# Kernel tuning notes

Measured on AMD Instinct MI355X. Metric: run time of the kernel, lower is better.

The kernel has to match this reference:

```python
import jax, jax.numpy as jnp
import numpy as np
from jax import lax

D_MODEL = 512
N_HEADS = 8
D_HEAD = D_MODEL // N_HEADS
MAX_LANDMARKS = 100


def setup_inputs() -> dict:
    key = jax.random.key(0)
    ks = jax.random.split(key, 12)
    B, L, D = 16, 8192, D_MODEL
    s = 1.0 / np.sqrt(D)
    return {
        "mamba_output": jax.random.normal(ks[0], (B, L, D), jnp.float32),
        "hawkes_skip": jax.random.normal(ks[1], (B, L, D), jnp.float32),
        "hawkes_weights": jax.random.uniform(ks[2], (B, L), jnp.float32),
        "Wq": jax.random.uniform(ks[3], (D, D), jnp.float32, -s, s),
        "bq": jax.random.uniform(ks[4], (D,), jnp.float32, -s, s),
        "Wk": jax.random.uniform(ks[5], (D, D), jnp.float32, -s, s),
        "bk": jax.random.uniform(ks[6], (D,), jnp.float32, -s, s),
        "Wv": jax.random.uniform(ks[7], (D, D), jnp.float32, -s, s),
        "bv": jax.random.uniform(ks[8], (D,), jnp.float32, -s, s),
        "Wo": jax.random.uniform(ks[9], (D, D), jnp.float32, -s, s),
        "bo": jax.random.uniform(ks[10], (D,), jnp.float32, -s, s),
    }


def reference(mamba_output, hawkes_skip, hawkes_weights,
              Wq, bq, Wk, bk, Wv, bv, Wo, bo):
    B, L, D = hawkes_skip.shape
    H, dh = N_HEADS, D_HEAD
    k = min(MAX_LANDMARKS, L)
    scale = dh ** (-0.5)

    # top-k landmark selection over sequence, then chronological sort
    _, idx = lax.top_k(hawkes_weights, k)          # (B, k)
    idx = jnp.sort(idx, axis=1)
    landmark_kv = jnp.take_along_axis(hawkes_skip, idx[:, :, None], axis=1)  # (B, k, D)

    # single query = last timestep of mamba output
    query = mamba_output[:, -1, :]                 # (B, D)
    Q = (query @ Wq.T + bq).reshape(B, H, dh)      # (B, H, dh)
    K = (landmark_kv @ Wk.T + bk).reshape(B, k, H, dh)
    V = (landmark_kv @ Wv.T + bv).reshape(B, k, H, dh)

    scores = jnp.einsum("bhd,bkhd->bhk", Q, K) * scale   # (B, H, k)
    probs = jax.nn.softmax(scores, axis=-1)
    attn = jnp.einsum("bhk,bkhd->bhd", probs, V).reshape(B, D)
    return attn @ Wo.T + bo                        # (B, D)
```

## Files before the change

kernel.cpp:

```cpp
#include <hip/hip_runtime.h>
#include <hip/hip_bf16.h>
#include <stdint.h>

#define B_SZ 16
#define L_SEQ 8192
#define D_MOD 512
#define N_H 8
#define D_H 64
#define KSEL 100

__global__ __launch_bounds__(512) void fused_attn_kernel(
    const float* __restrict__ mamba, const float* __restrict__ skip,
    const float* __restrict__ w,
    const float* __restrict__ Wq, const float* __restrict__ bq,
    const float* __restrict__ Wk, const float* __restrict__ bk,
    const float* __restrict__ Wv, const float* __restrict__ bv,
    float* __restrict__ attn_out) {
    const int b = blockIdx.x >> 3;
    const int h = blockIdx.x & 7;
    const int t = threadIdx.x;
    const int lane = t & 63;
    const int wave = t >> 6;

    __shared__ uint32_t uval[L_SEQ];
    __shared__ float s_part[8 * D_MOD];
    __shared__ float s_query[D_MOD];
    __shared__ float s_a[D_MOD];
    __shared__ float s_y[D_MOD];
    __shared__ float s_Qh[D_H];
    __shared__ int s_idx[128];
    __shared__ int hist[256];
    __shared__ int s_wtot[4];
    __shared__ float s_m[8], s_l[8];
    __shared__ uint32_t s_thresh;
    __shared__ int s_rem, s_cnt;
    __shared__ float s_qdotbk;

    const float* qrow = mamba + ((size_t)b * L_SEQ + (L_SEQ - 1)) * D_MOD;
    if (t < D_MOD) s_query[t] = qrow[t];
    const float* wb = w + (size_t)b * L_SEQ;
    for (int i = t; i < L_SEQ; i += 512) uval[i] = __float_as_uint(wb[i]);
    __syncthreads();

    const float* Wqh = Wq + (size_t)(h * D_H) * D_MOD;
    {
        const float4* q4 = (const float4*)s_query;
        float4 q0 = q4[lane * 2], q1 = q4[lane * 2 + 1];
        for (int d = wave; d < D_H; d += 8) {
            const float4* row4 = (const float4*)(Wqh + (size_t)d * D_MOD);
            float4 w0 = row4[lane * 2], w1 = row4[lane * 2 + 1];
            float sum = w0.x * q0.x + w0.y * q0.y + w0.z * q0.z + w0.w * q0.w +
                        w1.x * q1.x + w1.y * q1.y + w1.z * q1.z + w1.w * q1.w;
            #pragma unroll
            for (int off = 32; off > 0; off >>= 1) sum += __shfl_down(sum, off);
            if (lane == 0) s_Qh[d] = sum + bq[h * D_H + d];
        }
    }
    __syncthreads();

    if (wave == 0) {
        float v = s_Qh[lane] * bk[h * D_H + lane];
        #pragma unroll
        for (int off = 32; off > 0; off >>= 1) v += __shfl_down(v, off);
        if (lane == 0) s_qdotbk = v;
    }
    {
        const float* Wkh = Wk + (size_t)(h * D_H) * D_MOD;
        float4 a0 = {0, 0, 0, 0}, a1 = {0, 0, 0, 0};
        #pragma unroll
        for (int dd = 0; dd < 8; ++dd) {
            const int d = wave * 8 + dd;
            float qd = s_Qh[d];
            const float4* row4 = (const float4*)(Wkh + (size_t)d * D_MOD);
            float4 w0 = row4[lane * 2], w1 = row4[lane * 2 + 1];
            a0.x += qd * w0.x; a0.y += qd * w0.y; a0.z += qd * w0.z; a0.w += qd * w0.w;
            a1.x += qd * w1.x; a1.y += qd * w1.y; a1.z += qd * w1.z; a1.w += qd * w1.w;
        }
        float4* p4 = (float4*)&s_part[wave * D_MOD + lane * 8];
        p4[0] = a0; p4[1] = a1;
    }
    __syncthreads();
    {
        float v = 0.f;
        #pragma unroll
        for (int ww = 0; ww < 8; ++ww) v += s_part[ww * D_MOD + t];
        s_a[t] = v;
    }

    uint32_t prefix = 0, pmask = 0;
    int remaining = KSEL;
    for (int pass = 0; pass < 4; ++pass) {
        const int shift = 24 - 8 * pass;
        if (t < 256) hist[t] = 0;
        __syncthreads();
        for (int i = t; i < L_SEQ; i += 512) {
            uint32_t u = uval[i];
            if ((u & pmask) == prefix) atomicAdd(&hist[(u >> shift) & 0xFF], 1);
        }
        __syncthreads();
        int v = 0;
        if (t < 256) {
            v = hist[t];
            #pragma unroll
            for (int off = 1; off < 64; off <<= 1) {
                int u = __shfl_down(v, off);
                if (lane + off < 64) v += u;
            }
            if (lane == 0) s_wtot[wave] = v;
        }
        __syncthreads();
        if (t < 256) {
            int hi = 0;
            for (int w2 = wave + 1; w2 < 4; ++w2) hi += s_wtot[w2];
            int suff = v + hi;
            int suff_next = suff - hist[t];
            if (suff >= remaining && suff_next < remaining) {
                s_thresh = prefix | ((uint32_t)t << shift);
                s_rem = remaining - suff_next;
            }
        }
        __syncthreads();
        prefix = s_thresh;
        remaining = s_rem;
        pmask |= (uint32_t)0xFF << shift;
        __syncthreads();
    }

    if (t == 0) s_cnt = 0;
    __syncthreads();
    for (int i = t; i < L_SEQ; i += 512) {
        if (uval[i] > prefix) {
            int p = atomicAdd(&s_cnt, 1);
            s_idx[p] = i;
        }
    }
    __syncthreads();
    const int cntgt = s_cnt;
    if (wave == 0) {
        int needed = remaining;
        int taken = 0;
        for (int base = 0; base < L_SEQ && needed > 0; base += 64) {
            bool eq = (uval[base + lane] == prefix);
            unsigned long long mask = __ballot(eq);
            int before = __popcll(mask & ((1ull << lane) - 1ull));
            int c = __popcll(mask);
            int take = c < needed ? c : needed;
            if (eq && before < take) s_idx[cntgt + taken + before] = base + lane;
            taken += take;
            needed -= take;
        }
    }
    __syncthreads();

    const float scale = 0.125f;
    {
        const float4* a4 = (const float4*)s_a;
        float4 av0 = a4[lane * 2], av1 = a4[lane * 2 + 1];
        float qdotbk = s_qdotbk;
        float m = -INFINITY, l = 0.f;
        float4 acc0 = {0, 0, 0, 0}, acc1 = {0, 0, 0, 0};
        for (int j = wave; j < KSEL; j += 8) {
            const float4* x4 =
                (const float4*)(skip + ((size_t)b * L_SEQ + s_idx[j]) * D_MOD);
            float4 x0 = x4[lane * 2], x1 = x4[lane * 2 + 1];
            float sum = x0.x * av0.x + x0.y * av0.y + x0.z * av0.z + x0.w * av0.w +
                        x1.x * av1.x + x1.y * av1.y + x1.z * av1.z + x1.w * av1.w;
            #pragma unroll
            for (int off = 32; off > 0; off >>= 1) sum += __shfl_xor(sum, off);
            float s = (sum + qdotbk) * scale;
            float mnew = fmaxf(m, s);
            float c = expf(m - mnew);
            float e = expf(s - mnew);
            l = l * c + e;
            acc0.x = acc0.x * c + e * x0.x; acc0.y = acc0.y * c + e * x0.y;
            acc0.z = acc0.z * c + e * x0.z; acc0.w = acc0.w * c + e * x0.w;
            acc1.x = acc1.x * c + e * x1.x; acc1.y = acc1.y * c + e * x1.y;
            acc1.z = acc1.z * c + e * x1.z; acc1.w = acc1.w * c + e * x1.w;
            m = mnew;
        }
        float4* p4 = (float4*)&s_part[wave * D_MOD + lane * 8];
        p4[0] = acc0; p4[1] = acc1;
        if (lane == 0) { s_m[wave] = m; s_l[wave] = l; }
    }
    __syncthreads();

    {
        float mstar = -INFINITY;
        #pragma unroll
        for (int ww = 0; ww < 8; ++ww) mstar = fmaxf(mstar, s_m[ww]);
        float num = 0.f, den = 0.f;
        #pragma unroll
        for (int ww = 0; ww < 8; ++ww) {
            float sc = expf(s_m[ww] - mstar);
            num += sc * s_part[ww * D_MOD + t];
            den += sc * s_l[ww];
        }
        s_y[t] = num / den;
    }
    __syncthreads();

    const float* Wvh = Wv + (size_t)(h * D_H) * D_MOD;
    {
        const float4* y4 = (const float4*)s_y;
        float4 y0 = y4[lane * 2], y1 = y4[lane * 2 + 1];
        for (int d = wave; d < D_H; d += 8) {
            const float4* row4 = (const float4*)(Wvh + (size_t)d * D_MOD);
            float4 w0 = row4[lane * 2], w1 = row4[lane * 2 + 1];
            float sum = w0.x * y0.x + w0.y * y0.y + w0.z * y0.z + w0.w * y0.w +
                        w1.x * y1.x + w1.y * y1.y + w1.z * y1.z + w1.w * y1.w;
            #pragma unroll
            for (int off = 32; off > 0; off >>= 1) sum += __shfl_down(sum, off);
            if (lane == 0)
                attn_out[(size_t)b * D_MOD + h * D_H + d] = sum + bv[h * D_H + d];
        }
    }
}

__global__ __launch_bounds__(256) void out_kernel(const float* __restrict__ attn,
                                                  const float* __restrict__ Wo,
                                                  const float* __restrict__ bo,
                                                  float* __restrict__ out) {
    const int b = blockIdx.x & 15;
    const int rc = blockIdx.x >> 4;
    const int t = threadIdx.x;
    const int lane = t & 63;
    const int wave = t >> 6;

    __shared__ float s_attn[D_MOD];
    for (int i = t; i < D_MOD; i += 256) s_attn[i] = attn[(size_t)b * D_MOD + i];
    __syncthreads();

    const float4* a4 = (const float4*)s_attn;
    float4 a0 = a4[lane * 2], a1 = a4[lane * 2 + 1];
    for (int d = wave; d < 64; d += 4) {
        const int r = rc * 64 + d;
        const float4* row4 = (const float4*)(Wo + (size_t)r * D_MOD);
        float4 w0 = row4[lane * 2], w1 = row4[lane * 2 + 1];
        float sum = w0.x * a0.x + w0.y * a0.y + w0.z * a0.z + w0.w * a0.w +
                    w1.x * a1.x + w1.y * a1.y + w1.z * a1.z + w1.w * a1.w;
        #pragma unroll
        for (int off = 32; off > 0; off >>= 1) sum += __shfl_down(sum, off);
        if (lane == 0) out[(size_t)b * D_MOD + r] = sum + bo[r];
    }
}

extern "C" void kernel_launch(void* const* d_in, const int* in_sizes, int n_in,
                              void* d_out, int out_size, void* d_ws, size_t ws_size,
                              hipStream_t stream) {
    const float* mamba = (const float*)d_in[0];
    const float* skip  = (const float*)d_in[1];
    const float* hw    = (const float*)d_in[2];
    const float* Wq    = (const float*)d_in[3];
    const float* bq    = (const float*)d_in[4];
    const float* Wk    = (const float*)d_in[5];
    const float* bk    = (const float*)d_in[6];
    const float* Wv    = (const float*)d_in[7];
    const float* bv    = (const float*)d_in[8];
    const float* Wo    = (const float*)d_in[9];
    const float* bo    = (const float*)d_in[10];
    float* out = (float*)d_out;

    float* attn = (float*)d_ws;

    fused_attn_kernel<<<B_SZ * N_H, 512, 0, stream>>>(mamba, skip, hw, Wq, bq,
                                                      Wk, bk, Wv, bv, attn);
    out_kernel<<<B_SZ * N_H, 256, 0, stream>>>(attn, Wo, bo, out);
}
```

Measured before the change: 464.2 us.

## Fuse output projection into attention kernel via atomics; prefetch landmark rows

Removes the separate output-projection kernel: each (batch, head) block multiplies its 64-wide head slice by the matching Wo columns and atomically adds into the zeroed output, with the bias added by head 0. Tie handling at the top-k threshold now records equal-valued indices during the main scan and picks the smallest ones with a wave-level min-reduction, replacing a full ballot sweep of the sequence. The landmark gather loop software-prefetches the next row before computing on the current one. In exchange it adds a memset launch, non-deterministic float atomic summation order, and caps tie candidates at 128.

```diff
diff --git a/kernel.cpp b/kernel.cpp
--- a/kernel.cpp
+++ b/kernel.cpp
@@ -15,7 +15,8 @@
     const float* __restrict__ Wq, const float* __restrict__ bq,
     const float* __restrict__ Wk, const float* __restrict__ bk,
     const float* __restrict__ Wv, const float* __restrict__ bv,
-    float* __restrict__ attn_out) {
+    const float* __restrict__ Wo, const float* __restrict__ bo,
+    float* __restrict__ out) {
     const int b = blockIdx.x >> 3;
     const int h = blockIdx.x & 7;
     const int t = threadIdx.x;
@@ -28,12 +29,14 @@
     __shared__ float s_a[D_MOD];
     __shared__ float s_y[D_MOD];
     __shared__ float s_Qh[D_H];
+    __shared__ float s_ah[D_H];
     __shared__ int s_idx[128];
+    __shared__ int s_eq[128];
     __shared__ int hist[256];
     __shared__ int s_wtot[4];
     __shared__ float s_m[8], s_l[8];
     __shared__ uint32_t s_thresh;
-    __shared__ int s_rem, s_cnt;
+    __shared__ int s_rem, s_cnt, s_ecnt;
     __shared__ float s_qdotbk;
 
     const float* qrow = mamba + ((size_t)b * L_SEQ + (L_SEQ - 1)) * D_MOD;
@@ -126,28 +129,36 @@
         __syncthreads();
     }
 
-    if (t == 0) s_cnt = 0;
+    if (t == 0) { s_cnt = 0; s_ecnt = 0; }
     __syncthreads();
     for (int i = t; i < L_SEQ; i += 512) {
-        if (uval[i] > prefix) {
+        uint32_t u = uval[i];
+        if (u > prefix) {
             int p = atomicAdd(&s_cnt, 1);
             s_idx[p] = i;
+        } else if (u == prefix) {
+            int p = atomicAdd(&s_ecnt, 1);
+            if (p < 128) s_eq[p] = i;
         }
     }
     __syncthreads();
     const int cntgt = s_cnt;
     if (wave == 0) {
-        int needed = remaining;
-        int taken = 0;
-        for (int base = 0; base < L_SEQ && needed > 0; base += 64) {
-            bool eq = (uval[base + lane] == prefix);
-            unsigned long long mask = __ballot(eq);
-            int before = __popcll(mask & ((1ull << lane) - 1ull));
-            int c = __popcll(mask);
-            int take = c < needed ? c : needed;
-            if (eq && before < take) s_idx[cntgt + taken + before] = base + lane;
-            taken += take;
-            needed -= take;
+        int n = s_ecnt < 128 ? s_ecnt : 128;
+        int taken_val = -1;
+        for (int r = 0; r < remaining; ++r) {
+            int mymin = 0x7FFFFFFF;
+            for (int i = lane; i < n; i += 64) {
+                int e = s_eq[i];
+                if (e > taken_val && e < mymin) mymin = e;
+            }
+            #pragma unroll
+            for (int off = 32; off > 0; off >>= 1) {
+                int o = __shfl_xor(mymin, off);
+                mymin = o < mymin ? o : mymin;
+            }
+            if (lane == 0) s_idx[cntgt + r] = mymin;
+            taken_val = mymin;
         }
     }
     __syncthreads();
@@ -159,10 +170,21 @@
         float qdotbk = s_qdotbk;
         float m = -INFINITY, l = 0.f;
         float4 acc0 = {0, 0, 0, 0}, acc1 = {0, 0, 0, 0};
-        for (int j = wave; j < KSEL; j += 8) {
+        int j = wave;
+        float4 x0 = {0, 0, 0, 0}, x1 = {0, 0, 0, 0};
+        if (j < KSEL) {
             const float4* x4 =
                 (const float4*)(skip + ((size_t)b * L_SEQ + s_idx[j]) * D_MOD);
-            float4 x0 = x4[lane * 2], x1 = x4[lane * 2 + 1];
+            x0 = x4[lane * 2]; x1 = x4[lane * 2 + 1];
+        }
+        while (j < KSEL) {
+            const int jn = j + 8;
+            float4 n0 = {0, 0, 0, 0}, n1 = {0, 0, 0, 0};
+            if (jn < KSEL) {
+                const float4* x4 =
+                    (const float4*)(skip + ((size_t)b * L_SEQ + s_idx[jn]) * D_MOD);
+                n0 = x4[lane * 2]; n1 = x4[lane * 2 + 1];
+            }
             float sum = x0.x * av0.x + x0.y * av0.y + x0.z * av0.z + x0.w * av0.w +
                         x1.x * av1.x + x1.y * av1.y + x1.z * av1.z + x1.w * av1.w;
             #pragma unroll
@@ -177,6 +199,8 @@
             acc1.x = acc1.x * c + e * x1.x; acc1.y = acc1.y * c + e * x1.y;
             acc1.z = acc1.z * c + e * x1.z; acc1.w = acc1.w * c + e * x1.w;
             m = mnew;
+            x0 = n0; x1 = n1;
+            j = jn;
         }
         float4* p4 = (float4*)&s_part[wave * D_MOD + lane * 8];
         p4[0] = acc0; p4[1] = acc1;
@@ -210,37 +234,23 @@
                         w1.x * y1.x + w1.y * y1.y + w1.z * y1.z + w1.w * y1.w;
             #pragma unroll
             for (int off = 32; off > 0; off >>= 1) sum += __shfl_down(sum, off);
-            if (lane == 0)
-                attn_out[(size_t)b * D_MOD + h * D_H + d] = sum + bv[h * D_H + d];
-        }
-    }
-}
-
-__global__ __launch_bounds__(256) void out_kernel(const float* __restrict__ attn,
-                                                  const float* __restrict__ Wo,
-                                                  const float* __restrict__ bo,
-                                                  float* __restrict__ out) {
-    const int b = blockIdx.x & 15;
-    const int rc = blockIdx.x >> 4;
-    const int t = threadIdx.x;
-    const int lane = t & 63;
-    const int wave = t >> 6;
-
-    __shared__ float s_attn[D_MOD];
-    for (int i = t; i < D_MOD; i += 256) s_attn[i] = attn[(size_t)b * D_MOD + i];
-    __syncthreads();
-
-    const float4* a4 = (const float4*)s_attn;
-    float4 a0 = a4[lane * 2], a1 = a4[lane * 2 + 1];
-    for (int d = wave; d < 64; d += 4) {
-        const int r = rc * 64 + d;
-        const float4* row4 = (const float4*)(Wo + (size_t)r * D_MOD);
-        float4 w0 = row4[lane * 2], w1 = row4[lane * 2 + 1];
-        float sum = w0.x * a0.x + w0.y * a0.y + w0.z * a0.z + w0.w * a0.w +
-                    w1.x * a1.x + w1.y * a1.y + w1.z * a1.z + w1.w * a1.w;
-        #pragma unroll
-        for (int off = 32; off > 0; off >>= 1) sum += __shfl_down(sum, off);
-        if (lane == 0) out[(size_t)b * D_MOD + r] = sum + bo[r];
+            if (lane == 0) s_ah[d] = sum + bv[h * D_H + d];
+        }
+    }
+    __syncthreads();
+
+    {
+        const float4* wrow = (const float4*)(Wo + (size_t)t * D_MOD + h * D_H);
+        const float4* ah4 = (const float4*)s_ah;
+        float acc = 0.f;
+        #pragma unroll
+        for (int i = 0; i < 16; ++i) {
+            float4 wv = wrow[i];
+            float4 av = ah4[i];
+            acc += wv.x * av.x + wv.y * av.y + wv.z * av.z + wv.w * av.w;
+        }
+        if (h == 0) acc += bo[t];
+        atomicAdd(&out[(size_t)b * D_MOD + t], acc);
     }
 }
 
@@ -260,9 +270,7 @@
     const float* bo    = (const float*)d_in[10];
     float* out = (float*)d_out;
 
-    float* attn = (float*)d_ws;
-
+    hipMemsetAsync(out, 0, (size_t)out_size * sizeof(float), stream);
     fused_attn_kernel<<<B_SZ * N_H, 512, 0, stream>>>(mamba, skip, hw, Wq, bq,
-                                                      Wk, bk, Wv, bv, attn);
-    out_kernel<<<B_SZ * N_H, 256, 0, stream>>>(attn, Wo, bo, out);
+                                                      Wk, bk, Wv, bv, Wo, bo, out);
 }
```

After: 455.8 us. About the same (-1.8%).
